# Performance work log

Measured on AMD Instinct MI355X. Metric: run time of the kernel, lower is better.

## Reference

```python
import jax, jax.numpy as jnp
import numpy as np

NUM_HEADS = 8
NUM_Q = 64
RANK = 64
DIM = 768
LN_EPS = 1e-5


def setup_inputs() -> dict:
    key = jax.random.key(0)
    ks = jax.random.split(key, 8)
    b, n = 4, 1024
    x = jax.random.normal(ks[0], (b, NUM_Q, DIM), dtype=jnp.float32)
    context = jax.random.normal(ks[1], (b, n, DIM), dtype=jnp.float32)
    s = 0.02
    Wq = jax.random.normal(ks[2], (DIM, DIM), dtype=jnp.float32) * s
    Wk = jax.random.normal(ks[3], (DIM, DIM), dtype=jnp.float32) * s
    Wv1 = jax.random.normal(ks[4], (DIM, NUM_Q * RANK), dtype=jnp.float32) * s
    ln_g = jnp.ones((NUM_Q * RANK,), dtype=jnp.float32)
    ln_b = jnp.zeros((NUM_Q * RANK,), dtype=jnp.float32)
    Wc = jax.random.normal(ks[5], (NUM_Q, RANK, DIM), dtype=jnp.float32) * s
    Wout = jax.random.normal(ks[6], (DIM, DIM), dtype=jnp.float32) * s
    return {"x": x, "context": context, "Wq": Wq, "Wk": Wk, "Wv1": Wv1,
            "ln_g": ln_g, "ln_b": ln_b, "Wc": Wc, "Wout": Wout}


def reference(x, context, Wq, Wk, Wv1, ln_g, ln_b, Wc, Wout):
    b, nq, d = x.shape
    n = context.shape[1]
    h, dh = NUM_HEADS, d // NUM_HEADS

    q = x @ Wq                      # [b, nq, d]
    k = context @ Wk                # [b, n, d]

    # q-aware V: Linear -> LayerNorm(all_q_mid) -> grouped 1x1 conv (per-query rank->d)
    h1 = context @ Wv1              # [b, n, NUM_Q*RANK]
    mu = jnp.mean(h1, axis=-1, keepdims=True)
    var = jnp.var(h1, axis=-1, keepdims=True)
    h1 = (h1 - mu) * jax.lax.rsqrt(var + LN_EPS) * ln_g + ln_b
    vmid = h1.reshape(b, n, NUM_Q, RANK)
    v = jnp.einsum('bnqr,qrd->bqnd', vmid, Wc)   # [b, NUM_Q, n, d]
    # split heads: 'b q n (h dh) -> b h q n dh'
    v = v.reshape(b, NUM_Q, n, h, dh).transpose(0, 3, 1, 2, 4)

    qh = q.reshape(b, nq, h, dh).transpose(0, 2, 1, 3)   # [b,h,nq,dh]
    kh = k.reshape(b, n, h, dh).transpose(0, 2, 1, 3)    # [b,h,n,dh]
    scale = dh ** (-0.25)
    sim = jnp.einsum('bhid,bhjd->bhij', qh * scale, kh * scale)
    attn = jax.nn.softmax(sim, axis=-1)                  # [b,h,nq,n]
    out = jnp.einsum('bhij,bhijd->bhid', attn, v)        # per-query V
    out = out.transpose(0, 2, 1, 3).reshape(b, nq, d)
    return out @ Wout
```

## Files before the change

### kernel.cpp

```cpp
#include <hip/hip_runtime.h>
#include <math.h>

typedef unsigned short ushort_t;
typedef __bf16 bf16x8 __attribute__((ext_vector_type(8)));
typedef float f32x4 __attribute__((ext_vector_type(4)));

__device__ __forceinline__ ushort_t f2b_rne(float f) {
    union { float f; unsigned int u; } c;
    c.f = f;
    unsigned int u = c.u;
    u += 0x7FFFu + ((u >> 16) & 1u);
    return (ushort_t)(u >> 16);
}
__device__ __forceinline__ float b2f(ushort_t v) {
    union { unsigned int u; float f; } c;
    c.u = ((unsigned int)v) << 16;
    return c.f;
}

__device__ __forceinline__ void gl_lds16(const ushort_t* g, ushort_t* l) {
    __builtin_amdgcn_global_load_lds(
        (const __attribute__((address_space(1))) void*)g,
        (__attribute__((address_space(3))) void*)l, 16, 0, 0);
}

__global__ __launch_bounds__(256) void prep(
    const float* __restrict__ x, const float* __restrict__ context,
    const float* __restrict__ Wq, const float* __restrict__ Wk,
    const float* __restrict__ Wv1, const float* __restrict__ Wout,
    ushort_t* __restrict__ x_b, ushort_t* __restrict__ ctx_b,
    ushort_t* __restrict__ Wq_t, ushort_t* __restrict__ Wk_t,
    ushort_t* __restrict__ Wv1_t, ushort_t* __restrict__ Wout_b,
    float* __restrict__ colzero,
    int b, int n) {
    const int t = threadIdx.x;
    const int bid = blockIdx.x;
    const int nb_x = (b * 64 * 768 / 4) / 256;
    const int nb_c = (b * n * 768 / 4) / 256;

    if (bid < nb_x + nb_c) {
        const float* in = (bid < nb_x) ? x : context;
        ushort_t* outp = (bid < nb_x) ? x_b : ctx_b;
        const int i = ((bid < nb_x) ? bid : (bid - nb_x)) * 256 + t;
        float4 v = ((const float4*)in)[i];
        ushort_t o[4] = {f2b_rne(v.x), f2b_rne(v.y), f2b_rne(v.z), f2b_rne(v.w)};
        *(uint2*)&outp[(size_t)i * 4] = *(uint2*)o;
        return;
    }

    int u = bid - nb_x - nb_c;
    if (u >= 1632) {
        const int idx = (u - 1632) * 256 + t;
        ((float4*)colzero)[idx] = make_float4(0.f, 0.f, 0.f, 0.f);
        return;
    }
    if (u >= 1056) {
        const int i = (u - 1056) * 256 + t;
        float4 v = ((const float4*)Wout)[i];
        ushort_t o[4] = {f2b_rne(v.x), f2b_rne(v.y), f2b_rne(v.z), f2b_rne(v.w)};
        *(uint2*)&Wout_b[(size_t)i * 4] = *(uint2*)o;
        return;
    }

    const float* in;
    ushort_t* outp;
    int R = 768, C = 768;
    if (u < 144)        { in = Wq;  outp = Wq_t; }
    else if (u < 288)   { u -= 144; in = Wk;  outp = Wk_t; }
    else                { u -= 288; in = Wv1; outp = Wv1_t; C = 4096; }
    const int ct = C / 64;
    const int c0 = (u % ct) * 64, r0 = (u / ct) * 64;

    __shared__ float tt[64][65];
    const int lr = t >> 4;
    const int lc = (t & 15) * 4;
#pragma unroll
    for (int i = 0; i < 4; i++) {
        const float4 v =
            *(const float4*)&in[(size_t)(r0 + lr + 16 * i) * C + c0 + lc];
        tt[lr + 16 * i][lc + 0] = v.x;
        tt[lr + 16 * i][lc + 1] = v.y;
        tt[lr + 16 * i][lc + 2] = v.z;
        tt[lr + 16 * i][lc + 3] = v.w;
    }
    __syncthreads();
    const int rr = (t & 15) * 4;
    const int cc = t >> 4;
#pragma unroll
    for (int i = 0; i < 4; i++) {
        const int col = cc + 16 * i;
        ushort_t o[4] = {f2b_rne(tt[rr + 0][col]), f2b_rne(tt[rr + 1][col]),
                         f2b_rne(tt[rr + 2][col]), f2b_rne(tt[rr + 3][col])};
        *(uint2*)&outp[(size_t)(c0 + col) * R + r0 + rr] = *(uint2*)o;
    }
}

__device__ __forceinline__ void gemm_tile_big(
    const ushort_t* __restrict__ A, const ushort_t* __restrict__ Bt,
    ushort_t* __restrict__ C, int N, int row0, int col0, ushort_t* lds) {
    constexpr int K = 768;
    constexpr int NSTEP = 24;
    constexpr int SLOT = 512 * 32;

    const int t = threadIdx.x;
    const int lane = t & 63, wave = t >> 6;
    const int quad = lane >> 4, l15 = lane & 15;
    const int wm = (wave >> 2) * 128;
    const int wn = (wave & 3) * 64;

    const int srow = lane >> 2;
    const int sslot = (lane & 3) ^ ((lane >> 3) & 3);
    const ushort_t* gA = A + (size_t)(row0 + wave * 32 + srow) * K + sslot * 8;
    const ushort_t* gB = Bt + (size_t)(col0 + wave * 32 + srow) * K + sslot * 8;
    const int ldsA = wave * 1024;
    const int ldsB = 256 * 32 + wave * 1024;

    const int rslot = (quad ^ ((l15 >> 1) & 3)) * 8;
    const int abase = (wm + l15) * 32 + rslot;
    const int bbase = 256 * 32 + (wn + l15) * 32 + rslot;

    f32x4 acc[8][4] = {};
    bf16x8 af[8], bfr[4];

    auto STAGE_A = [&](int s) {
        const int rg = (s & 3) * SLOT;
        const int ko = s * 32;
        gl_lds16(gA + ko, lds + rg + ldsA);
        gl_lds16(gA + 16 * K + ko, lds + rg + ldsA + 512);
    };
    auto STAGE_B = [&](int s) {
        const int rg = (s & 3) * SLOT;
        const int ko = s * 32;
        gl_lds16(gB + ko, lds + rg + ldsB);
        gl_lds16(gB + 16 * K + ko, lds + rg + ldsB + 512);
    };
    auto READ_B = [&](int s) {
        const ushort_t* p = lds + (s & 3) * SLOT + bbase;
#pragma unroll
        for (int j = 0; j < 4; ++j) bfr[j] = *(const bf16x8*)&p[j * 512];
    };
    auto READ_A_LO = [&](int s) {
        const ushort_t* p = lds + (s & 3) * SLOT + abase;
#pragma unroll
        for (int i = 0; i < 4; ++i) af[i] = *(const bf16x8*)&p[i * 512];
    };
    auto READ_A_HI = [&](int s) {
        const ushort_t* p = lds + (s & 3) * SLOT + abase;
#pragma unroll
        for (int i = 4; i < 8; ++i) af[i] = *(const bf16x8*)&p[i * 512];
    };
    auto MFMA_LO = [&]() {
        __builtin_amdgcn_s_setprio(1);
#pragma unroll
        for (int i = 0; i < 4; ++i)
#pragma unroll
            for (int j = 0; j < 4; ++j)
                acc[i][j] = __builtin_amdgcn_mfma_f32_16x16x32_bf16(
                    af[i], bfr[j], acc[i][j], 0, 0, 0);
        __builtin_amdgcn_s_setprio(0);
    };
    auto MFMA_HI = [&]() {
        __builtin_amdgcn_s_setprio(1);
#pragma unroll
        for (int i = 4; i < 8; ++i)
#pragma unroll
            for (int j = 0; j < 4; ++j)
                acc[i][j] = __builtin_amdgcn_mfma_f32_16x16x32_bf16(
                    af[i], bfr[j], acc[i][j], 0, 0, 0);
        __builtin_amdgcn_s_setprio(0);
    };

    STAGE_A(0); STAGE_B(0);
    STAGE_A(1); STAGE_B(1);
    STAGE_A(2); STAGE_B(2);
    asm volatile("s_waitcnt vmcnt(8)" ::: "memory");
    __builtin_amdgcn_s_barrier();

    for (int s = 0; s < NSTEP - 3; ++s) {
        READ_B(s);
        READ_A_LO(s);
        STAGE_A(s + 3);
        __builtin_amdgcn_sched_barrier(0);
        __builtin_amdgcn_s_barrier();
        asm volatile("s_waitcnt lgkmcnt(0)" ::: "memory");
        __builtin_amdgcn_sched_barrier(0);
        MFMA_LO();
        __builtin_amdgcn_sched_barrier(0);
        __builtin_amdgcn_s_barrier();
        READ_A_HI(s);
        STAGE_B(s + 3);
        asm volatile("s_waitcnt vmcnt(8)" ::: "memory");
        __builtin_amdgcn_sched_barrier(0);
        __builtin_amdgcn_s_barrier();
        asm volatile("s_waitcnt lgkmcnt(0)" ::: "memory");
        __builtin_amdgcn_sched_barrier(0);
        MFMA_HI();
        __builtin_amdgcn_sched_barrier(0);
        __builtin_amdgcn_s_barrier();
    }

    asm volatile("s_waitcnt vmcnt(0)" ::: "memory");
    __builtin_amdgcn_s_barrier();
#pragma unroll
    for (int s = NSTEP - 3; s < NSTEP; ++s) {
        READ_B(s);
        READ_A_LO(s);
        READ_A_HI(s);
        asm volatile("s_waitcnt lgkmcnt(0)" ::: "memory");
        __builtin_amdgcn_sched_barrier(0);
        MFMA_LO();
        MFMA_HI();
    }

#pragma unroll
    for (int i = 0; i < 8; ++i)
#pragma unroll
        for (int j = 0; j < 4; ++j)
#pragma unroll
            for (int r = 0; r < 4; ++r) {
                const int row = row0 + wm + i * 16 + quad * 4 + r;
                const int col = col0 + wn + j * 16 + l15;
                C[(size_t)row * N + col] = f2b_rne(acc[i][j][r]);
            }
}

__device__ __forceinline__ void gemm_tile_small(
    const ushort_t* __restrict__ A, const ushort_t* __restrict__ Bt,
    ushort_t* __restrict__ C, int N, int row0, int col0, ushort_t* lds) {
    constexpr int K = 768;
    constexpr int NSTEP = 24;
    constexpr int SLOT = 256 * 32;

    const int t = threadIdx.x;
    const int lane = t & 63, wave = t >> 6;
    const int quad = lane >> 4, l15 = lane & 15;
    const int wm = (wave >> 2) * 64;
    const int wn = (wave & 3) * 32;

    const int srow = lane >> 2;
    const int sslot = (lane & 3) ^ ((lane >> 3) & 3);
    const ushort_t* gA = A + (size_t)(row0 + wave * 16 + srow) * K + sslot * 8;
    const ushort_t* gB = Bt + (size_t)(col0 + wave * 16 + srow) * K + sslot * 8;
    const int ldsA = wave * 512;
    const int ldsB = 128 * 32 + wave * 512;

    const int rslot = (quad ^ ((l15 >> 1) & 3)) * 8;
    const int abase = (wm + l15) * 32 + rslot;
    const int bbase = 128 * 32 + (wn + l15) * 32 + rslot;

    f32x4 acc[4][2] = {};

    auto STAGE = [&](int s) {
        const int rg = (s & 3) * SLOT;
        const int ko = s * 32;
        gl_lds16(gA + ko, lds + rg + ldsA);
        gl_lds16(gB + ko, lds + rg + ldsB);
    };

    auto COMPUTE = [&](int s) {
        const int rg = (s & 3) * SLOT;
        const ushort_t* pA = lds + rg + abase;
        const ushort_t* pB = lds + rg + bbase;
        bf16x8 af[4], bfr[2];
#pragma unroll
        for (int i = 0; i < 4; ++i) af[i] = *(const bf16x8*)&pA[i * 512];
#pragma unroll
        for (int j = 0; j < 2; ++j) bfr[j] = *(const bf16x8*)&pB[j * 512];
        __builtin_amdgcn_s_setprio(1);
#pragma unroll
        for (int i = 0; i < 4; ++i)
#pragma unroll
            for (int j = 0; j < 2; ++j)
                acc[i][j] = __builtin_amdgcn_mfma_f32_16x16x32_bf16(
                    af[i], bfr[j], acc[i][j], 0, 0, 0);
        __builtin_amdgcn_s_setprio(0);
    };

    STAGE(0); STAGE(1); STAGE(2);

    for (int s = 0; s < NSTEP - 3; ++s) {
        __builtin_amdgcn_sched_barrier(0);
        __builtin_amdgcn_s_barrier();
        STAGE(s + 3);
        asm volatile("s_waitcnt vmcnt(6)" ::: "memory");
        __builtin_amdgcn_s_barrier();
        __builtin_amdgcn_sched_barrier(0);
        COMPUTE(s);
    }
    __builtin_amdgcn_sched_barrier(0);
    __builtin_amdgcn_s_barrier();
    asm volatile("s_waitcnt vmcnt(0)" ::: "memory");
    __builtin_amdgcn_s_barrier();
    __builtin_amdgcn_sched_barrier(0);
    COMPUTE(NSTEP - 3);
    COMPUTE(NSTEP - 2);
    COMPUTE(NSTEP - 1);

#pragma unroll
    for (int i = 0; i < 4; ++i)
#pragma unroll
        for (int j = 0; j < 2; ++j)
#pragma unroll
            for (int r = 0; r < 4; ++r) {
                const int row = row0 + wm + i * 16 + quad * 4 + r;
                const int col = col0 + wn + j * 16 + l15;
                C[(size_t)row * N + col] = f2b_rne(acc[i][j][r]);
            }
}

__global__ __launch_bounds__(512, 2) void gemm_ring(
    const ushort_t* __restrict__ x_b, const ushort_t* __restrict__ ctx_b,
    const ushort_t* __restrict__ Wq_t, const ushort_t* __restrict__ Wk_t,
    const ushort_t* __restrict__ Wv1_t,
    ushort_t* __restrict__ qb, ushort_t* __restrict__ kb,
    ushort_t* __restrict__ h1t, int b, int n) {
    extern __shared__ ushort_t lds[];
    const int Mn = b * n;
    const int M = b * 64;
    const int nbig = 16 * (Mn / 256);
    const int nk = (Mn / 128) * 6;
    int u = blockIdx.x;
    if (u < nbig) {
        gemm_tile_big(Wv1_t, ctx_b, h1t, Mn, (u & 15) * 256, (u >> 4) * 256,
                      lds);
    } else if ((u -= nbig) < nk) {
        const int rt = Mn / 128;
        gemm_tile_small(ctx_b, Wk_t, kb, 768, (u % rt) * 128, (u / rt) * 128,
                        lds);
    } else {
        u -= nk;
        const int rt = M / 128;
        gemm_tile_small(x_b, Wq_t, qb, 768, (u % rt) * 128, (u / rt) * 128,
                        lds);
    }
}

__global__ __launch_bounds__(256) void scores_stats(
    const ushort_t* __restrict__ qb, const ushort_t* __restrict__ kb,
    const ushort_t* __restrict__ h1t, float* __restrict__ S,
    float* __restrict__ colsum, float* __restrict__ colsumsq,
    int b, int n, int Mn) {
    __shared__ ushort_t sb[192 * 104];
    const int t = threadIdx.x;
    const int nsc = b * 8 * (n / 128);

    if (blockIdx.x >= nsc) {
        const int u = blockIdx.x - nsc;
        const int rc = u >> 4;
        const int cc = u & 15;
        const int cg = t & 31;
        const int rg = t >> 5;
        const ushort_t* p =
            h1t + (size_t)(rc * 256 + rg * 32) * Mn + cc * 256 + cg * 8;
        float s[8] = {}, s2[8] = {};
#pragma unroll 4
        for (int r = 0; r < 32; r++) {
            const bf16x8 v = *(const bf16x8*)&p[(size_t)r * Mn];
#pragma unroll
            for (int j = 0; j < 8; j++) {
                const float f = (float)v[j];
                s[j] += f;
                s2[j] += f * f;
            }
        }
        float* red = (float*)sb;
#pragma unroll
        for (int j = 0; j < 8; j++) {
            red[rg * 256 + cg * 8 + j] = s[j];
            red[2048 + rg * 256 + cg * 8 + j] = s2[j];
        }
        __syncthreads();
        float ts = 0.f, ts2 = 0.f;
#pragma unroll
        for (int g = 0; g < 8; g++) {
            ts += red[g * 256 + t];
            ts2 += red[2048 + g * 256 + t];
        }
        atomicAdd(&colsum[cc * 256 + t], ts);
        atomicAdd(&colsumsq[cc * 256 + t], ts2);
        return;
    }

    const int nt = n / 128;
    const int n0 = (blockIdx.x % nt) * 128;
    const int bh = blockIdx.x / nt;
    const int bb = bh >> 3, h = bh & 7;
    const int lane = t & 63, wave = t >> 6;
    const int quad = lane >> 4, l15 = lane & 15;
    const int wm = (wave >> 1) * 32;
    const int wn = (wave & 1) * 64;

    ushort_t* Qs = sb;
    ushort_t* Ks = sb + 64 * 104;

    for (int g = t; g < 768; g += 256) {
        const int r = g / 12, s = g - r * 12;
        *(bf16x8*)&Qs[r * 104 + s * 8] =
            *(const bf16x8*)&qb[(size_t)(bb * 64 + r) * 768 + h * 96 + s * 8];
    }
    for (int g = t; g < 1536; g += 256) {
        const int r = g / 12, s = g - r * 12;
        *(bf16x8*)&Ks[r * 104 + s * 8] =
            *(const bf16x8*)&kb[(size_t)(bb * n + n0 + r) * 768 + h * 96 + s * 8];
    }
    __syncthreads();

    f32x4 acc[2][4] = {};
#pragma unroll
    for (int ks = 0; ks < 3; ks++) {
        bf16x8 af[2], bfr[4];
#pragma unroll
        for (int i = 0; i < 2; i++)
            af[i] = *(const bf16x8*)&Qs[(wm + i * 16 + l15) * 104 + ks * 32 + quad * 8];
#pragma unroll
        for (int j = 0; j < 4; j++)
            bfr[j] = *(const bf16x8*)&Ks[(wn + j * 16 + l15) * 104 + ks * 32 + quad * 8];
#pragma unroll
        for (int i = 0; i < 2; i++)
#pragma unroll
            for (int j = 0; j < 4; j++)
                acc[i][j] = __builtin_amdgcn_mfma_f32_16x16x32_bf16(
                    af[i], bfr[j], acc[i][j], 0, 0, 0);
    }

    const float sc = 0.10206207261596575f;
    float* Sp = S + (size_t)bh * 64 * n;
#pragma unroll
    for (int i = 0; i < 2; i++)
#pragma unroll
        for (int j = 0; j < 4; j++)
#pragma unroll
            for (int r = 0; r < 4; r++) {
                const int row = wm + i * 16 + quad * 4 + r;
                const int col = n0 + wn + j * 16 + l15;
                Sp[(size_t)row * n + col] = acc[i][j][r] * sc;
            }
}

__global__ __launch_bounds__(1024) void attn_fused(
    const float* __restrict__ S, const float* __restrict__ colsum,
    const float* __restrict__ colsumsq, const ushort_t* __restrict__ h1t,
    const float* __restrict__ ln_g, const float* __restrict__ ln_b,
    const float* __restrict__ Wc, const ushort_t* __restrict__ Wout_b,
    float* __restrict__ out, int n, int Mn) {
    const int bq = blockIdx.x;
    const int bb = bq >> 6, qi = bq & 63;
    const int tid = threadIdx.x;
    const int lane = tid & 63, wv = tid >> 6;
    const int quad = lane >> 4, l15 = lane & 15;

    __shared__ ushort_t sW[9 * 1032];
    __shared__ ushort_t sH[64 * 264];
    __shared__ float sl[8], swmu[8];
    __shared__ float pm[16], pl[16], pwm[16];
    __shared__ float sA[512];
    __shared__ float sO[768];

    float* sMu = (float*)sH;
    float* sRs = (float*)sH + 1024;

    for (int i = tid; i < n; i += 1024) {
        const float cs = colsum[bb * n + i];
        const float cq = colsumsq[bb * n + i];
        const float m = cs * (1.0f / 4096.0f);
        sMu[i] = m;
        sRs[i] = rsqrtf(cq * (1.0f / 4096.0f) - m * m + 1e-5f);
    }
    for (int i = tid; i < 1032; i += 1024) sW[8 * 1032 + i] = 0;
    __syncthreads();

    const int h = wv >> 1;
    const int half = wv & 1;
    const int nh = n >> 1;
    const int i0 = half * nh;
    const float* Sp = S + ((size_t)(bb * 8 + h) * 64 + qi) * n;
    {
        float m = -1e30f;
        for (int i = i0 + lane; i < i0 + nh; i += 64) m = fmaxf(m, Sp[i]);
#pragma unroll
        for (int off = 32; off > 0; off >>= 1) m = fmaxf(m, __shfl_down(m, off));
        if (lane == 0) pm[wv] = m;
    }
    __syncthreads();
    const float mh = fmaxf(pm[2 * h], pm[2 * h + 1]);
    {
        float l = 0.f, wm = 0.f;
        for (int i = i0 + lane; i < i0 + nh; i += 64) {
            const float e = expf(Sp[i] - mh);
            const float w = e * sRs[i];
            const ushort_t wb = f2b_rne(w);
            sW[h * 1032 + i] = wb;
            l += e;
            wm += b2f(wb) * sMu[i];
        }
#pragma unroll
        for (int off = 32; off > 0; off >>= 1) {
            l += __shfl_down(l, off);
            wm += __shfl_down(wm, off);
        }
        if (lane == 0) { pl[wv] = l; pwm[wv] = wm; }
    }
    __syncthreads();
    if (tid < 8) {
        sl[tid] = pl[2 * tid] + pl[2 * tid + 1];
        swmu[tid] = pwm[2 * tid] + pwm[2 * tid + 1];
    }

    const int mrow = (l15 < 8 ? l15 : 8) * 1032;
    f32x4 acc = {};
    const int nch = n >> 8;
    for (int ch = 0; ch < nch; ch++) {
        __syncthreads();
        for (int g = tid; g < 2048; g += 1024) {
            const int row = g >> 5, seg = g & 31;
            *(bf16x8*)&sH[row * 264 + seg * 8] =
                *(const bf16x8*)&h1t[(size_t)(qi * 64 + row) * Mn + bb * n +
                                     ch * 256 + seg * 8];
        }
        __syncthreads();
        if (wv < 4) {
#pragma unroll
            for (int ks = 0; ks < 8; ks++) {
                const bf16x8 af = *(const bf16x8*)&sW[mrow + ch * 256 + ks * 32 + quad * 8];
                const bf16x8 bf = *(const bf16x8*)&sH[(wv * 16 + l15) * 264 + ks * 32 + quad * 8];
                acc = __builtin_amdgcn_mfma_f32_16x16x32_bf16(af, bf, acc, 0, 0, 0);
            }
        }
    }
    __syncthreads();

    if (wv < 4) {
#pragma unroll
        for (int r = 0; r < 4; r++) {
            const int hh = quad * 4 + r;
            if (hh < 8) {
                const int rr = wv * 16 + l15;
                const int c = qi * 64 + rr;
                sA[hh * 64 + rr] =
                    ln_g[c] * ((acc[r] - swmu[hh]) / sl[hh]) + ln_b[c];
            }
        }
    }
    __syncthreads();

    for (int d = tid; d < 768; d += 1024) {
        const int hh = d / 96;
        const float* wp = Wc + (size_t)qi * 49152 + d;
        float a = 0.f;
#pragma unroll
        for (int r = 0; r < 64; r++) a += sA[hh * 64 + r] * wp[(size_t)r * 768];
        sO[d] = b2f(f2b_rne(a));
    }
    __syncthreads();

    float* rbuf = (float*)sH;
    if (tid < 768) {
        const int r0 = tid / 96;
        const int c0 = (tid % 96) * 8;
        const ushort_t* wp = Wout_b + (size_t)(r0 * 96) * 768 + c0;
        float acc8[8] = {};
#pragma unroll 4
        for (int s = 0; s < 96; s++) {
            const float sv = sO[r0 * 96 + s];
            const bf16x8 w8 = *(const bf16x8*)&wp[(size_t)s * 768];
#pragma unroll
            for (int j = 0; j < 8; j++) acc8[j] += sv * (float)w8[j];
        }
#pragma unroll
        for (int j = 0; j < 8; j++) rbuf[r0 * 768 + c0 + j] = acc8[j];
    }
    __syncthreads();
    if (tid < 768) {
        float s = 0.f;
#pragma unroll
        for (int g = 0; g < 8; g++) s += rbuf[g * 768 + tid];
        out[(size_t)bq * 768 + tid] = s;
    }
}

extern "C" void kernel_launch(void* const* d_in, const int* in_sizes, int n_in,
                              void* d_out, int out_size, void* d_ws, size_t ws_size,
                              hipStream_t stream) {
    const float* x       = (const float*)d_in[0];
    const float* context = (const float*)d_in[1];
    const float* Wq      = (const float*)d_in[2];
    const float* Wk      = (const float*)d_in[3];
    const float* Wv1     = (const float*)d_in[4];
    const float* ln_g    = (const float*)d_in[5];
    const float* ln_b    = (const float*)d_in[6];
    const float* Wc      = (const float*)d_in[7];
    const float* Wout    = (const float*)d_in[8];
    float* out = (float*)d_out;

    const int b = in_sizes[0] / (64 * 768);
    const int n = in_sizes[1] / (b * 768);
    const int M  = b * 64;
    const int Mn = b * n;

    float* ws = (float*)d_ws;
    size_t off = 0;
    float* S       = ws + off;  off += (size_t)b * 8 * 64 * n;
    float* colsum  = ws + off;  off += (size_t)Mn;
    float* colsumsq= ws + off;  off += (size_t)Mn;

    ushort_t* us = (ushort_t*)(ws + off);
    size_t uo = 0;
    ushort_t* x_b    = us + uo;  uo += (size_t)M * 768;
    ushort_t* ctx_b  = us + uo;  uo += (size_t)Mn * 768;
    ushort_t* qb     = us + uo;  uo += (size_t)M * 768;
    ushort_t* kb     = us + uo;  uo += (size_t)Mn * 768;
    ushort_t* h1t    = us + uo;  uo += (size_t)Mn * 4096;
    ushort_t* Wq_t   = us + uo;  uo += (size_t)768 * 768;
    ushort_t* Wk_t   = us + uo;  uo += (size_t)768 * 768;
    ushort_t* Wv1_t  = us + uo;  uo += (size_t)4096 * 768;
    ushort_t* Wout_b = us + uo;  uo += (size_t)768 * 768;

    const int nb_x = (M * 768 / 4) / 256;
    const int nb_c = (Mn * 768 / 4) / 256;
    prep<<<nb_x + nb_c + 1640, 256, 0, stream>>>(
        x, context, Wq, Wk, Wv1, Wout, x_b, ctx_b, Wq_t, Wk_t, Wv1_t, Wout_b,
        colsum, b, n);

    const int nbig = 16 * (Mn / 256);
    const int nk = (Mn / 128) * 6;
    const int nq = (M / 128) * 6;
    static bool attr_done = false;
    if (!attr_done) {
        (void)hipFuncSetAttribute(reinterpret_cast<const void*>(&gemm_ring),
                                  hipFuncAttributeMaxDynamicSharedMemorySize,
                                  131072);
        attr_done = true;
    }
    gemm_ring<<<nbig + nk + nq, 512, 131072, stream>>>(
        x_b, ctx_b, Wq_t, Wk_t, Wv1_t, qb, kb, h1t, b, n);

    scores_stats<<<b * 8 * (n / 128) + 256, 256, 0, stream>>>(
        qb, kb, h1t, S, colsum, colsumsq, b, n, Mn);

    attn_fused<<<M, 1024, 0, stream>>>(S, colsum, colsumsq, h1t, ln_g, ln_b,
                                       Wc, Wout_b, out, n, Mn);
}
```

Before: 167.8 us.

## Split attention-weighted reduction over sequence across all 16 waves with LDS reduce

Replaces the chunked loop, where only 4 of 16 waves ran MFMAs after staging h1t tiles into LDS, with a split-K scheme: each wave loads its B fragments directly from global memory for one 256-wide slice of n, then partial accumulators are summed through LDS. This removes the per-chunk LDS staging and barriers and uses all waves for the MFMA work. The slice mapping is hardcoded to four slices of 256, so it assumes n equals 1024 rather than looping over n>>8, and the direct global fragment loads may be less coalesced.

Result: no change. 167.5 us (-0.2%).

```diff
diff --git a/kernel.cpp b/kernel.cpp
--- a/kernel.cpp
+++ b/kernel.cpp
@@ -507,29 +507,34 @@
     }
 
     const int mrow = (l15 < 8 ? l15 : 8) * 1032;
+    const int jb = wv & 3;
+    const int kg = wv >> 2;
     f32x4 acc = {};
-    const int nch = n >> 8;
-    for (int ch = 0; ch < nch; ch++) {
-        __syncthreads();
-        for (int g = tid; g < 2048; g += 1024) {
-            const int row = g >> 5, seg = g & 31;
-            *(bf16x8*)&sH[row * 264 + seg * 8] =
-                *(const bf16x8*)&h1t[(size_t)(qi * 64 + row) * Mn + bb * n +
-                                     ch * 256 + seg * 8];
-        }
-        __syncthreads();
-        if (wv < 4) {
-#pragma unroll
-            for (int ks = 0; ks < 8; ks++) {
-                const bf16x8 af = *(const bf16x8*)&sW[mrow + ch * 256 + ks * 32 + quad * 8];
-                const bf16x8 bf = *(const bf16x8*)&sH[(wv * 16 + l15) * 264 + ks * 32 + quad * 8];
-                acc = __builtin_amdgcn_mfma_f32_16x16x32_bf16(af, bf, acc, 0, 0, 0);
-            }
-        }
-    }
+    {
+        const ushort_t* hp =
+            h1t + (size_t)(qi * 64 + jb * 16 + l15) * Mn + bb * n + kg * 256 +
+            quad * 8;
+        const ushort_t* wp = sW + mrow + kg * 256 + quad * 8;
+#pragma unroll
+        for (int ks = 0; ks < 8; ks++) {
+            const bf16x8 af = *(const bf16x8*)&wp[ks * 32];
+            const bf16x8 bf = *(const bf16x8*)&hp[ks * 32];
+            acc = __builtin_amdgcn_mfma_f32_16x16x32_bf16(af, bf, acc, 0, 0, 0);
+        }
+    }
+    __syncthreads();
+    float* red = (float*)sH;
+    *(f32x4*)&red[(size_t)(wv * 64 + lane) * 4] = acc;
     __syncthreads();
 
     if (wv < 4) {
+        f32x4 a = *(const f32x4*)&red[(size_t)(wv * 64 + lane) * 4];
+#pragma unroll
+        for (int g = 1; g < 4; g++) {
+            const f32x4 p = *(const f32x4*)&red[(size_t)((g * 4 + wv) * 64 + lane) * 4];
+#pragma unroll
+            for (int r = 0; r < 4; r++) a[r] += p[r];
+        }
 #pragma unroll
         for (int r = 0; r < 4; r++) {
             const int hh = quad * 4 + r;
@@ -537,7 +542,7 @@
                 const int rr = wv * 16 + l15;
                 const int c = qi * 64 + rr;
                 sA[hh * 64 + rr] =
-                    ln_g[c] * ((acc[r] - swmu[hh]) / sl[hh]) + ln_b[c];
+                    ln_g[c] * ((a[r] - swmu[hh]) / sl[hh]) + ln_b[c];
             }
         }
     }
```
